# Kernel tuning notes

Measured on AMD Instinct MI355X. Metric: run time of the kernel, lower is better.

The kernel has to match this reference:

```python
import jax, jax.numpy as jnp
import numpy as np
import math

B, L, C, H, CP = 2, 512, 576, 8, 128
C3 = C // 3            # 192
DK = C // H            # 72
DK3 = DK // 3          # 24
DIV = math.sqrt(DK)


def _ln(x, w, b, eps=1e-6):
    m = jnp.mean(x, axis=-1, keepdims=True)
    v = jnp.mean(jnp.square(x - m), axis=-1, keepdims=True)
    return (x - m) * jax.lax.rsqrt(v + eps) * w + b


def setup_inputs() -> dict:
    key = jax.random.key(0)
    ks = jax.random.split(key, 12)
    s = 0.05
    def n(k, shape):
        return jax.random.normal(k, shape, jnp.float32) * s
    return {
        "x": jax.random.normal(ks[0], (B, L, C), jnp.float32),
        "pairX": jax.random.normal(ks[1], (B, L, L, CP), jnp.float32),
        "g": jnp.ones((1,), jnp.float32),
        "ln1_w": jnp.ones((C,), jnp.float32), "ln1_b": jnp.zeros((C,), jnp.float32),
        "ln2_w": jnp.ones((CP,), jnp.float32), "ln2_b": jnp.zeros((CP,), jnp.float32),
        "Wq": n(ks[2], (C3, C3)), "bq": jnp.zeros((C3,), jnp.float32),
        "Wk": n(ks[3], (C3, C3)), "bk": jnp.zeros((C3,), jnp.float32),
        "Wv": n(ks[4], (C3, C3)), "bv": jnp.zeros((C3,), jnp.float32),
        "Wg": n(ks[5], (C3, C3)), "bg": jnp.zeros((C3,), jnp.float32),
        "conv_w": n(ks[6], (3, H, H, 5, 5)), "conv_b": jnp.zeros((3, H), jnp.float32),
        "Wp": n(ks[7], (CP, H)), "bp": jnp.zeros((H,), jnp.float32),
        "Wpr": n(ks[8], (H, CP)), "bpr": jnp.zeros((CP,), jnp.float32),
        "Wo": n(ks[9], (C, C)), "bo": jnp.zeros((C,), jnp.float32),
    }


def reference(x, pairX, g, ln1_w, ln1_b, ln2_w, ln2_b, Wq, bq, Wk, bk, Wv, bv,
              Wg, bg, conv_w, conv_b, Wp, bp, Wpr, bpr, Wo, bo):
    ori_x = x
    xn = _ln(x, ln1_w, ln1_b)                      # [B,L,C]
    pn = _ln(pairX, ln2_w, ln2_b)                  # [B,L,L,CP]

    # split channels into 3 groups: [B,3,L,C3]
    xs = xn.reshape(B, L, 3, C3).transpose(0, 2, 1, 3)

    def proj(W, b):
        y = xs @ W + b                              # [B,3,L,C3]
        return y.reshape(B, 3, L, H, DK3).transpose(0, 1, 3, 2, 4)  # [B,3,H,L,DK3]

    q = proj(Wq, bq)
    k = proj(Wk, bk)
    v = proj(Wv, bv)
    gate = proj(Wg, bg)

    qkMatrix = jnp.einsum('bchld,bchmd->bchlm', q, k)  # [B,3,H,L,L]
    pairBias = (pn @ Wp + bp).transpose(0, 3, 1, 2)[:, None]  # [B,1,H,L,L]
    oriQK = qkMatrix + pairBias                     # [B,3,H,L,L]

    # 3-channel 5x5 conv refinement, summed over the 3 branches -> [B,1,H,L,L]
    dn = ('NCHW', 'OIHW', 'NCHW')
    convQK = sum(
        jax.lax.conv_general_dilated(oriQK[:, i], conv_w[i], (1, 1), 'SAME',
                                     dimension_numbers=dn)
        + conv_b[i][None, :, None, None]
        for i in range(3)
    )[:, None]

    qk = (oriQK + convQK) / DIV                     # [B,3,H,L,L]
    score = jax.nn.softmax(qk, axis=-1)
    h_outs = jnp.einsum('bchlm,bchmd->bchld', score, v) * jax.nn.sigmoid(gate)
    h_outs = h_outs.transpose(0, 3, 1, 2, 4).reshape(B, L, C)

    rawScoreMean = jax.nn.gelu(jnp.mean(qk, axis=1).transpose(0, 2, 3, 1),
                               approximate=False)   # [B,L,L,H]
    out1 = (h_outs @ Wo + bo) + ori_x * g
    out2 = rawScoreMean @ Wpr + bpr                 # [B,L,L,CP]
    return out1, out2
```

## Files before the change

### kernel.cpp

```cpp
#include <hip/hip_runtime.h>
#include <hip/hip_bf16.h>

#define BDIM 2
#define LDIM 512
#define CDIM 576
#define HDIM 8
#define CPD  128
#define DK3  24
#define INV_DIV 0.117851130197757920f

static constexpr size_t OFF_Q    = 0;
static constexpr size_t OFF_K    = 589824;
static constexpr size_t OFF_V    = 1179648;
static constexpr size_t OFF_G    = 1769472;
static constexpr size_t OFF_BIAS = 2359296;
static constexpr size_t OFF_ORI  = OFF_BIAS + 4194304;
static constexpr size_t OFF_QK   = OFF_ORI + 12582912;
static constexpr size_t OFF_H    = OFF_QK + 12582912;
static constexpr size_t OFF_WPH  = OFF_H + 589824;
static constexpr size_t OFF_CS   = OFF_WPH + 1024;
static constexpr size_t OFF_XN   = OFF_QK;

__device__ __forceinline__ float gelu_exact(float v) {
    return 0.5f * v * (1.f + erff(v * 0.70710678118654752f));
}

typedef float __attribute__((ext_vector_type(4))) f32x4;
__device__ __forceinline__ void nt_store4(float* p, float a, float b, float c, float d) {
    f32x4 t = {a, b, c, d};
    __builtin_nontemporal_store(t, (f32x4*)p);
}

__global__ __launch_bounds__(256) void k_prep(
    const float* __restrict__ ln2w, const float* __restrict__ ln2b,
    const float* __restrict__ Wp, const float* __restrict__ bp,
    float* __restrict__ wph, float* __restrict__ csum)
{
    __shared__ float wl[1024];
    const int tid = threadIdx.x;
    for (int i = tid; i < 1024; i += 256) {
        int h = i >> 7, d = i & 127;
        float v = ln2w[d] * Wp[d * 8 + h];
        wl[i] = v; wph[i] = v;
    }
    __syncthreads();
    const int h = tid >> 5, c4 = tid & 31;
    float p = wl[h * 128 + c4 * 4] + wl[h * 128 + c4 * 4 + 1]
            + wl[h * 128 + c4 * 4 + 2] + wl[h * 128 + c4 * 4 + 3];
#pragma unroll
    for (int o = 1; o < 32; o <<= 1) p += __shfl_xor(p, o);
    if (c4 == 0) csum[h] = p;
    float q = 0.f;
#pragma unroll
    for (int k = 0; k < 4; ++k) { int d = c4 * 4 + k; q = fmaf(ln2b[d], Wp[d * 8 + h], q); }
#pragma unroll
    for (int o = 1; o < 32; o <<= 1) q += __shfl_xor(q, o);
    if (c4 == 0) csum[8 + h] = q + bp[h];
}

__global__ __launch_bounds__(256) void k_ln(
    const float* __restrict__ x, const float* __restrict__ ln1w, const float* __restrict__ ln1b,
    float* __restrict__ xn)
{
    const int tid = threadIdx.x;
    const int wid = tid >> 6, lane = tid & 63;
    const int row = blockIdx.x * 4 + wid;
    const float* xr = x + (size_t)row * CDIM;
    float vals[9]; float s = 0.f, sq = 0.f;
#pragma unroll
    for (int u = 0; u < 9; ++u) {
        float v = xr[lane + 64 * u];
        vals[u] = v; s += v; sq += v * v;
    }
#pragma unroll
    for (int o = 32; o; o >>= 1) { s += __shfl_xor(s, o); sq += __shfl_xor(sq, o); }
    float m = s * (1.f / 576.f);
    float inv = rsqrtf(sq * (1.f / 576.f) - m * m + 1e-6f);
    float* xo = xn + (size_t)row * CDIM;
#pragma unroll
    for (int u = 0; u < 9; ++u) {
        int idx = lane + 64 * u;
        xo[idx] = (vals[u] - m) * inv * ln1w[idx] + ln1b[idx];
    }
}

__global__ __launch_bounds__(256) void k_proj(
    const float* __restrict__ xn,
    const float* __restrict__ Wq, const float* __restrict__ bq,
    const float* __restrict__ Wk, const float* __restrict__ bk,
    const float* __restrict__ Wv, const float* __restrict__ bv,
    const float* __restrict__ Wg, const float* __restrict__ bg,
    float* __restrict__ qo, float* __restrict__ ko, float* __restrict__ vo, float* __restrict__ go)
{
    __shared__ float As[192 * 64];
    __shared__ float Bs[32 * 192];
    const int tid = threadIdx.x;
    const int bx = blockIdx.x;
    const int mi = bx / 48, rem = bx % 48;
    const int g = rem >> 4, rb = rem & 15;
    const int row0 = rb * 64;

    const float* W  = mi == 0 ? Wq : mi == 1 ? Wk : mi == 2 ? Wv : Wg;
    const float* bb = mi == 0 ? bq : mi == 1 ? bk : mi == 2 ? bv : bg;
    float* op       = mi == 0 ? qo : mi == 1 ? ko : mi == 2 ? vo : go;

    {
        const int r = tid & 63, k4b = tid >> 6;
#pragma unroll
        for (int it = 0; it < 12; ++it) {
            int k4 = k4b + it * 4;
            float4 v = *(const float4*)&xn[(size_t)(row0 + r) * 576 + g * 192 + k4 * 4];
            As[(k4 * 4 + 0) * 64 + r] = v.x;
            As[(k4 * 4 + 1) * 64 + r] = v.y;
            As[(k4 * 4 + 2) * 64 + r] = v.z;
            As[(k4 * 4 + 3) * 64 + r] = v.w;
        }
    }

    const int rg = tid >> 4, cg = tid & 15;
    const int r0 = rg * 4, c0 = cg * 12;
    float acc[4][12] = {};

    for (int kk = 0; kk < 192; kk += 32) {
        __syncthreads();
#pragma unroll
        for (int i = 0; i < 6; ++i) {
            int f = tid + 256 * i;
            int k2 = f / 48, c4 = f % 48;
            *(float4*)&Bs[k2 * 192 + c4 * 4] = *(const float4*)&W[(size_t)(kk + k2) * 192 + c4 * 4];
        }
        __syncthreads();
#pragma unroll
        for (int k2 = 0; k2 < 32; ++k2) {
            const float4 a  = *(const float4*)&As[(kk + k2) * 64 + r0];
            const float4 b0 = *(const float4*)&Bs[k2 * 192 + c0];
            const float4 b1 = *(const float4*)&Bs[k2 * 192 + c0 + 4];
            const float4 b2 = *(const float4*)&Bs[k2 * 192 + c0 + 8];
            const float ar[4] = {a.x, a.y, a.z, a.w};
#pragma unroll
            for (int r = 0; r < 4; ++r) {
                acc[r][0] = fmaf(ar[r], b0.x, acc[r][0]);
                acc[r][1] = fmaf(ar[r], b0.y, acc[r][1]);
                acc[r][2] = fmaf(ar[r], b0.z, acc[r][2]);
                acc[r][3] = fmaf(ar[r], b0.w, acc[r][3]);
                acc[r][4] = fmaf(ar[r], b1.x, acc[r][4]);
                acc[r][5] = fmaf(ar[r], b1.y, acc[r][5]);
                acc[r][6] = fmaf(ar[r], b1.z, acc[r][6]);
                acc[r][7] = fmaf(ar[r], b1.w, acc[r][7]);
                acc[r][8] = fmaf(ar[r], b2.x, acc[r][8]);
                acc[r][9] = fmaf(ar[r], b2.y, acc[r][9]);
                acc[r][10] = fmaf(ar[r], b2.z, acc[r][10]);
                acc[r][11] = fmaf(ar[r], b2.w, acc[r][11]);
            }
        }
    }

    const int h = cg >> 1, d24 = (cg & 1) * 12;
    const float4 bj0 = *(const float4*)&bb[c0];
    const float4 bj1 = *(const float4*)&bb[c0 + 4];
    const float4 bj2 = *(const float4*)&bb[c0 + 8];
#pragma unroll
    for (int r = 0; r < 4; ++r) {
        int row = row0 + r0 + r;
        int b = row >> 9, l = row & 511;
        float* o = op + ((((size_t)b * 3 + g) * HDIM + h) * LDIM + l) * DK3 + d24;
        *(float4*)(o + 0) = make_float4(acc[r][0] + bj0.x, acc[r][1] + bj0.y,
                                        acc[r][2] + bj0.z, acc[r][3] + bj0.w);
        *(float4*)(o + 4) = make_float4(acc[r][4] + bj1.x, acc[r][5] + bj1.y,
                                        acc[r][6] + bj1.z, acc[r][7] + bj1.w);
        *(float4*)(o + 8) = make_float4(acc[r][8] + bj2.x, acc[r][9] + bj2.y,
                                        acc[r][10] + bj2.z, acc[r][11] + bj2.w);
    }
}

__global__ __launch_bounds__(256) void k_pairbias(
    const float* __restrict__ pairX, const float* __restrict__ wph,
    const float* __restrict__ csum, float* __restrict__ bias)
{
    const int row = blockIdx.x * 256 + threadIdx.x;
    const float* rp = pairX + (size_t)row * CPD;

    float acc[8] = {};
    float sum = 0.f, sumsq = 0.f;
    for (int s = 0; s < 8; ++s) {
        float rr[16];
        *(float4*)&rr[0]  = *(const float4*)(rp + s * 16 + 0);
        *(float4*)&rr[4]  = *(const float4*)(rp + s * 16 + 4);
        *(float4*)&rr[8]  = *(const float4*)(rp + s * 16 + 8);
        *(float4*)&rr[12] = *(const float4*)(rp + s * 16 + 12);
#pragma unroll
        for (int k = 0; k < 16; ++k) { sum += rr[k]; sumsq = fmaf(rr[k], rr[k], sumsq); }
        const float* wp_s = wph + s * 16;
#pragma unroll
        for (int h = 0; h < 8; ++h) {
            const float* w = wp_s + h * 128;
#pragma unroll
            for (int k = 0; k < 16; ++k) acc[h] = fmaf(rr[k], w[k], acc[h]);
        }
    }
    const float m = sum * (1.f / 128.f);
    const float inv = rsqrtf(sumsq * (1.f / 128.f) - m * m + 1e-6f);
    const int b = row >> 18;
    const int ij = row & 262143;
    float* bo = bias + ((size_t)b << 21) + ij;
#pragma unroll
    for (int h = 0; h < 8; ++h) {
        float o = inv * (acc[h] - m * csum[h]) + csum[8 + h];
        bo[(size_t)h << 18] = o;
    }
}

__global__ __launch_bounds__(256) void k_qkmat(
    const float* __restrict__ q, const float* __restrict__ k,
    const float* __restrict__ bias, float* __restrict__ oriQK)
{
    __shared__ float Kl[512 * 28];
    __shared__ float Ql[32 * 28];
    const int tid = threadIdx.x;
    const int bch = blockIdx.x >> 4;
    const int itile = blockIdx.x & 15;
    const float* kp = k + (size_t)bch * 512 * 24;
    const float* qp = q + (size_t)bch * 512 * 24 + (size_t)itile * 32 * 24;
    for (int idx = tid; idx < 512 * 24; idx += 256) {
        int j = idx / 24, d = idx - j * 24;
        Kl[j * 28 + d] = kp[idx];
    }
    for (int idx = tid; idx < 32 * 24; idx += 256) {
        int i = idx / 24, d = idx - i * 24;
        Ql[i * 28 + d] = qp[idx];
    }
    __syncthreads();

    const int ti = tid >> 4, tj = tid & 15;
    const int b = bch / 24, h = bch & 7;
    const float* biasp = bias + ((size_t)(b * 8 + h) * 512 + itile * 32) * 512;
    float* outp = oriQK + (size_t)bch * 262144 + (size_t)itile * 32 * 512;

    for (int cc = 0; cc < 4; ++cc) {
        float acc[2][8] = {};
#pragma unroll
        for (int d4 = 0; d4 < 6; ++d4) {
            const float4 q0 = *(const float4*)&Ql[(ti * 2 + 0) * 28 + d4 * 4];
            const float4 q1 = *(const float4*)&Ql[(ti * 2 + 1) * 28 + d4 * 4];
#pragma unroll
            for (int u = 0; u < 8; ++u) {
                const float4 kv = *(const float4*)&Kl[(cc * 128 + u * 16 + tj) * 28 + d4 * 4];
                acc[0][u] = fmaf(q0.x, kv.x, fmaf(q0.y, kv.y, fmaf(q0.z, kv.z, fmaf(q0.w, kv.w, acc[0][u]))));
                acc[1][u] = fmaf(q1.x, kv.x, fmaf(q1.y, kv.y, fmaf(q1.z, kv.z, fmaf(q1.w, kv.w, acc[1][u]))));
            }
        }
#pragma unroll
        for (int r = 0; r < 2; ++r) {
            int i = ti * 2 + r;
#pragma unroll
            for (int u = 0; u < 8; ++u) {
                int j = cc * 128 + u * 16 + tj;
                outp[(size_t)i * 512 + j] = acc[r][u] + biasp[(size_t)i * 512 + j];
            }
        }
    }
}

__global__ __launch_bounds__(256, 4) void k_conv(
    const float* __restrict__ oriQK, const float* __restrict__ convW, const float* __restrict__ convB,
    const float* __restrict__ Wpr, const float* __restrict__ bpr,
    float* __restrict__ qk, float* __restrict__ out2)
{
    __shared__ float tile[8 * 36 * 24];
    __shared__ float wT[1600];
    const int tid = threadIdx.x;
    const int bx = blockIdx.x;
    const int b = bx >> 9, rem = bx & 511;
    const int i0 = (rem >> 5) * 32, j0 = (rem & 31) * 16;

    const int jg = tid & 7, ii = tid >> 3;
    const int j2 = jg * 2;
    float acc[8][2] = {};

    for (int c = 0; c < 3; ++c) {
        __syncthreads();
        for (int i = tid; i < 1600; i += 256) {
            int h = i & 7, rest = i >> 3;
            int tap = rest % 25, hi = rest / 25;
            wT[hi * 200 + tap * 8 + h] = convW[c * 1600 + h * 200 + hi * 25 + tap];
        }
        for (int idx = tid; idx < 8 * 720; idx += 256) {
            int ch = idx / 720;
            int r = idx - ch * 720;
            int iw = r / 20, jw = r - iw * 20;
            int gi = i0 - 2 + iw, gj = j0 - 2 + jw;
            float v = 0.f;
            if ((unsigned)gi < 512u && (unsigned)gj < 512u)
                v = oriQK[((size_t)(b * 24 + c * 8 + ch) << 18) + ((size_t)gi << 9) + gj];
            tile[ch * 864 + iw * 24 + jw] = v;
        }
        __syncthreads();

        for (int hi = 0; hi < 8; ++hi) {
            const float* tch = &tile[hi * 864];
            const float* wch = &wT[hi * 200];
#pragma unroll
            for (int kh = 0; kh < 5; ++kh) {
                const float* trow = &tch[(ii + kh) * 24 + j2];
                float v[6];
                *(float2*)&v[0] = *(const float2*)&trow[0];
                *(float2*)&v[2] = *(const float2*)&trow[2];
                *(float2*)&v[4] = *(const float2*)&trow[4];
#pragma unroll
                for (int kw = 0; kw < 5; ++kw) {
                    const float4 wA = *(const float4*)&wch[(kh * 5 + kw) * 8];
                    const float4 wB = *(const float4*)&wch[(kh * 5 + kw) * 8 + 4];
#pragma unroll
                    for (int j = 0; j < 2; ++j) {
                        float vv = v[kw + j];
                        acc[0][j] = fmaf(wA.x, vv, acc[0][j]);
                        acc[1][j] = fmaf(wA.y, vv, acc[1][j]);
                        acc[2][j] = fmaf(wA.z, vv, acc[2][j]);
                        acc[3][j] = fmaf(wA.w, vv, acc[3][j]);
                        acc[4][j] = fmaf(wB.x, vv, acc[4][j]);
                        acc[5][j] = fmaf(wB.y, vv, acc[5][j]);
                        acc[6][j] = fmaf(wB.z, vv, acc[6][j]);
                        acc[7][j] = fmaf(wB.w, vv, acc[7][j]);
                    }
                }
            }
        }
    }

    const int gi = i0 + ii, gj = j0 + j2;
    const float* orib = oriQK + ((size_t)(b * 24) << 18) + ((size_t)gi << 9) + gj;
    float* qkb = qk + ((size_t)(b * 24) << 18) + ((size_t)gi << 9) + gj;
#pragma unroll
    for (int h = 0; h < 8; ++h) {
        float cv = convB[h] + convB[8 + h] + convB[16 + h];
        float cj0 = acc[h][0] + cv, cj1 = acc[h][1] + cv;
        float mm0 = 0.f, mm1 = 0.f;
#pragma unroll
        for (int c = 0; c < 3; ++c) {
            const float2 t = *(const float2*)(orib + ((size_t)(c * 8 + h) << 18));
            mm0 += t.x; mm1 += t.y;
            float2 o = make_float2((t.x + cj0) * INV_DIV, (t.y + cj1) * INV_DIV);
            *(float2*)(qkb + ((size_t)(c * 8 + h) << 18)) = o;
        }
        acc[h][0] = gelu_exact((mm0 * (1.f / 3.f) + cj0) * INV_DIV);
        acc[h][1] = gelu_exact((mm1 * (1.f / 3.f) + cj1) * INV_DIV);
    }
    __syncthreads();

    float* gql = tile;
#pragma unroll
    for (int h = 0; h < 8; ++h)
        *(float2*)&gql[h * 512 + ii * 16 + j2] = make_float2(acc[h][0], acc[h][1]);
    __syncthreads();

    const int pq = tid & 31, pg = tid >> 5;
    float4 wv[8];
#pragma unroll
    for (int h = 0; h < 8; ++h) wv[h] = *(const float4*)&Wpr[h * 128 + pq * 4];
    const float4 bv = *(const float4*)&bpr[pq * 4];

    for (int it = 0; it < 64; ++it) {
        int pos = it * 8 + pg;
        float g8[8];
#pragma unroll
        for (int h = 0; h < 8; ++h) g8[h] = gql[h * 512 + pos];
        float ox = bv.x + g8[0]*wv[0].x + g8[1]*wv[1].x + g8[2]*wv[2].x + g8[3]*wv[3].x
                 + g8[4]*wv[4].x + g8[5]*wv[5].x + g8[6]*wv[6].x + g8[7]*wv[7].x;
        float oy = bv.y + g8[0]*wv[0].y + g8[1]*wv[1].y + g8[2]*wv[2].y + g8[3]*wv[3].y
                 + g8[4]*wv[4].y + g8[5]*wv[5].y + g8[6]*wv[6].y + g8[7]*wv[7].y;
        float oz = bv.z + g8[0]*wv[0].z + g8[1]*wv[1].z + g8[2]*wv[2].z + g8[3]*wv[3].z
                 + g8[4]*wv[4].z + g8[5]*wv[5].z + g8[6]*wv[6].z + g8[7]*wv[7].z;
        float ow = bv.w + g8[0]*wv[0].w + g8[1]*wv[1].w + g8[2]*wv[2].w + g8[3]*wv[3].w
                 + g8[4]*wv[4].w + g8[5]*wv[5].w + g8[6]*wv[6].w + g8[7]*wv[7].w;
        int oi = i0 + (pos >> 4), oj = j0 + (pos & 15);
        nt_store4(&out2[(((size_t)(b * 512 + oi) << 9) + oj) * 128 + pq * 4], ox, oy, oz, ow);
    }
}

__global__ __launch_bounds__(256) void k_softmax_pv(
    const float* __restrict__ qk, const float* __restrict__ v, const float* __restrict__ gate,
    float* __restrict__ houts)
{
    __shared__ float Vl[512 * 28];
    const int tid = threadIdx.x;
    const int bch = blockIdx.x >> 4, itile = blockIdx.x & 15;
    const float* vp = v + (size_t)bch * (512 * 24);
    for (int idx = tid; idx < 512 * 24; idx += 256) {
        int j = idx / 24, d = idx - j * 24;
        Vl[j * 28 + d] = vp[idx];
    }
    __syncthreads();

    const int wid = tid >> 6, lane = tid & 63;
    const int b = bch / 24, c = (bch % 24) >> 3, h = bch & 7;
    const int tg = lane >> 3;
    for (int rr = 0; rr < 8; ++rr) {
        const int i = itile * 32 + wid * 8 + rr;
        const float* row = qk + ((size_t)bch * 512 + i) * 512;
        float e[8]; float mx = -1e30f;
#pragma unroll
        for (int u = 0; u < 8; ++u) { e[u] = row[lane + 64 * u]; mx = fmaxf(mx, e[u]); }
#pragma unroll
        for (int o = 32; o; o >>= 1) mx = fmaxf(mx, __shfl_xor(mx, o));
        float s = 0.f;
#pragma unroll
        for (int u = 0; u < 8; ++u) { e[u] = __expf(e[u] - mx); s += e[u]; }
#pragma unroll
        for (int o = 32; o; o >>= 1) s += __shfl_xor(s, o);
        float inv = 1.f / s;

        float4 a4[6] = {};
#pragma unroll
        for (int u = 0; u < 8; ++u) {
            float p = e[u] * inv;
            const float* vr = &Vl[(u * 64 + lane) * 28];
#pragma unroll
            for (int k = 0; k < 6; ++k) {
                float4 vv = *(const float4*)(vr + 4 * k);
                a4[k].x = fmaf(p, vv.x, a4[k].x);
                a4[k].y = fmaf(p, vv.y, a4[k].y);
                a4[k].z = fmaf(p, vv.z, a4[k].z);
                a4[k].w = fmaf(p, vv.w, a4[k].w);
            }
        }
#pragma unroll
        for (int k = 0; k < 6; ++k) {
            a4[k].x += __shfl_xor(a4[k].x, 8);  a4[k].y += __shfl_xor(a4[k].y, 8);
            a4[k].z += __shfl_xor(a4[k].z, 8);  a4[k].w += __shfl_xor(a4[k].w, 8);
            a4[k].x += __shfl_xor(a4[k].x, 16); a4[k].y += __shfl_xor(a4[k].y, 16);
            a4[k].z += __shfl_xor(a4[k].z, 16); a4[k].w += __shfl_xor(a4[k].w, 16);
            a4[k].x += __shfl_xor(a4[k].x, 32); a4[k].y += __shfl_xor(a4[k].y, 32);
            a4[k].z += __shfl_xor(a4[k].z, 32); a4[k].w += __shfl_xor(a4[k].w, 32);
        }
        const float af[24] = {
            a4[0].x, a4[0].y, a4[0].z, a4[0].w, a4[1].x, a4[1].y, a4[1].z, a4[1].w,
            a4[2].x, a4[2].y, a4[2].z, a4[2].w, a4[3].x, a4[3].y, a4[3].z, a4[3].w,
            a4[4].x, a4[4].y, a4[4].z, a4[4].w, a4[5].x, a4[5].y, a4[5].z, a4[5].w };
        float w0 = tg==0?af[0]:tg==1?af[3]:tg==2?af[6]:tg==3?af[9]:tg==4?af[12]:tg==5?af[15]:tg==6?af[18]:af[21];
        float w1 = tg==0?af[1]:tg==1?af[4]:tg==2?af[7]:tg==3?af[10]:tg==4?af[13]:tg==5?af[16]:tg==6?af[19]:af[22];
        float w2 = tg==0?af[2]:tg==1?af[5]:tg==2?af[8]:tg==3?af[11]:tg==4?af[14]:tg==5?af[17]:tg==6?af[20]:af[23];
#pragma unroll
        for (int o = 1; o < 8; o <<= 1) {
            w0 += __shfl_xor(w0, o);
            w1 += __shfl_xor(w1, o);
            w2 += __shfl_xor(w2, o);
        }
        if ((lane & 7) == 0) {
            const int d0 = tg * 3;
            const float* gp = gate + ((size_t)bch * 512 + i) * 24 + d0;
            float* op = houts + ((size_t)(b * 512 + i)) * 576 + c * 192 + h * 24 + d0;
            op[0] = w0 / (1.f + __expf(-gp[0]));
            op[1] = w1 / (1.f + __expf(-gp[1]));
            op[2] = w2 / (1.f + __expf(-gp[2]));
        }
    }
}

__global__ __launch_bounds__(256) void k_out1(
    const float* __restrict__ houts, const float* __restrict__ Wo, const float* __restrict__ bo,
    const float* __restrict__ x, const float* __restrict__ gsc,
    float* __restrict__ out1)
{
    __shared__ float As[32 * 33];
    __shared__ float Bs[32 * 64];
    const int tid = threadIdx.x;
    const int mt = blockIdx.x / 9, nt = blockIdx.x % 9;
    const int m0 = mt * 32, n0 = nt * 64;
    const int tn = tid & 15, tm = tid >> 4;
    float acc[2][4] = {};

    for (int kk = 0; kk < 576; kk += 32) {
        {
            int idx = tid;
#pragma unroll
            for (int i = 0; i < 4; ++i, idx += 256) {
                int k2 = idx & 31, m = idx >> 5;
                As[m * 33 + k2] = houts[(size_t)(m0 + m) * 576 + kk + k2];
            }
        }
        {
            int idx = tid;
#pragma unroll
            for (int i = 0; i < 8; ++i, idx += 256) {
                int n = idx & 63, k2 = idx >> 6;
                Bs[k2 * 64 + n] = Wo[(size_t)(kk + k2) * 576 + n0 + n];
            }
        }
        __syncthreads();
#pragma unroll
        for (int k2 = 0; k2 < 32; ++k2) {
            float a0 = As[(tm * 2 + 0) * 33 + k2];
            float a1 = As[(tm * 2 + 1) * 33 + k2];
            const float4 bv = *(const float4*)&Bs[k2 * 64 + tn * 4];
            acc[0][0] += a0 * bv.x; acc[0][1] += a0 * bv.y; acc[0][2] += a0 * bv.z; acc[0][3] += a0 * bv.w;
            acc[1][0] += a1 * bv.x; acc[1][1] += a1 * bv.y; acc[1][2] += a1 * bv.z; acc[1][3] += a1 * bv.w;
        }
        __syncthreads();
    }

    const float gv = gsc[0];
    const float4 b4 = *(const float4*)&bo[n0 + tn * 4];
#pragma unroll
    for (int r = 0; r < 2; ++r) {
        size_t row = (size_t)m0 + tm * 2 + r;
        size_t off = row * 576 + n0 + tn * 4;
        const float4 x4 = *(const float4*)&x[off];
        nt_store4(&out1[off],
                  acc[r][0] + b4.x + x4.x * gv,
                  acc[r][1] + b4.y + x4.y * gv,
                  acc[r][2] + b4.z + x4.z * gv,
                  acc[r][3] + b4.w + x4.w * gv);
    }
}

extern "C" void kernel_launch(void* const* d_in, const int* in_sizes, int n_in,
                              void* d_out, int out_size, void* d_ws, size_t ws_size,
                              hipStream_t stream) {
    const float* x     = (const float*)d_in[0];
    const float* pairX = (const float*)d_in[1];
    const float* g     = (const float*)d_in[2];
    const float* ln1w  = (const float*)d_in[3];
    const float* ln1b  = (const float*)d_in[4];
    const float* ln2w  = (const float*)d_in[5];
    const float* ln2b  = (const float*)d_in[6];
    const float* Wq    = (const float*)d_in[7];
    const float* bq    = (const float*)d_in[8];
    const float* Wk    = (const float*)d_in[9];
    const float* bk    = (const float*)d_in[10];
    const float* Wv    = (const float*)d_in[11];
    const float* bv    = (const float*)d_in[12];
    const float* Wg    = (const float*)d_in[13];
    const float* bg    = (const float*)d_in[14];
    const float* convW = (const float*)d_in[15];
    const float* convB = (const float*)d_in[16];
    const float* Wp    = (const float*)d_in[17];
    const float* bp    = (const float*)d_in[18];
    const float* Wpr   = (const float*)d_in[19];
    const float* bpr   = (const float*)d_in[20];
    const float* Wo    = (const float*)d_in[21];
    const float* bo    = (const float*)d_in[22];

    float* ws   = (float*)d_ws;
    float* q    = ws + OFF_Q;
    float* k    = ws + OFF_K;
    float* vv   = ws + OFF_V;
    float* gt   = ws + OFF_G;
    float* bias = ws + OFF_BIAS;
    float* ori  = ws + OFF_ORI;
    float* qkb  = ws + OFF_QK;
    float* xn   = ws + OFF_XN;
    float* hout = ws + OFF_H;
    float* wph  = ws + OFF_WPH;
    float* csum = ws + OFF_CS;

    float* out1 = (float*)d_out;
    float* out2 = out1 + 589824;

    k_prep<<<dim3(1), dim3(256), 0, stream>>>(ln2w, ln2b, Wp, bp, wph, csum);
    k_ln<<<dim3(256), dim3(256), 0, stream>>>(x, ln1w, ln1b, xn);
    k_proj<<<dim3(192), dim3(256), 0, stream>>>(xn, Wq, bq, Wk, bk, Wv, bv, Wg, bg,
                                                q, k, vv, gt);
    k_pairbias<<<dim3(2048), dim3(256), 0, stream>>>(pairX, wph, csum, bias);
    k_qkmat<<<dim3(768), dim3(256), 0, stream>>>(q, k, bias, ori);
    k_conv<<<dim3(1024), dim3(256), 0, stream>>>(ori, convW, convB, Wpr, bpr, qkb, out2);
    k_softmax_pv<<<dim3(768), dim3(256), 0, stream>>>(qkb, vv, gt, hout);
    k_out1<<<dim3(288), dim3(256), 0, stream>>>(hout, Wo, bo, x, g, out1);
}
```

Before: 415.7 us.

## Defer qk materialization: store conv sum only and recompute logits in softmax

The conv kernel no longer writes the full 3-branch scaled qk tensor or re-reads oriQK from global memory. It takes the centre values for the branch mean from the shared tile it already loaded, and writes only the branch-summed conv output, which is a third of the size, into the now-dead pair-bias buffer. The softmax kernel rebuilds the logits as (ori + convsum) * 1/sqrt(dk) on load. This cuts global memory traffic, at the cost of an extra stream read in softmax and reliance on the bias buffer being dead after the qk-matrix kernel.

Result: slower. 424.4 us (+2.1%).

```diff
diff --git a/kernel.cpp b/kernel.cpp
--- a/kernel.cpp
+++ b/kernel.cpp
@@ -264,7 +264,7 @@
 __global__ __launch_bounds__(256, 4) void k_conv(
     const float* __restrict__ oriQK, const float* __restrict__ convW, const float* __restrict__ convB,
     const float* __restrict__ Wpr, const float* __restrict__ bpr,
-    float* __restrict__ qk, float* __restrict__ out2)
+    float* __restrict__ convsum, float* __restrict__ out2)
 {
     __shared__ float tile[8 * 36 * 24];
     __shared__ float wT[1600];
@@ -276,6 +276,7 @@
     const int jg = tid & 7, ii = tid >> 3;
     const int j2 = jg * 2;
     float acc[8][2] = {};
+    float mm[8][2] = {};
 
     for (int c = 0; c < 3; ++c) {
         __syncthreads();
@@ -325,25 +326,23 @@
                 }
             }
         }
+#pragma unroll
+        for (int h = 0; h < 8; ++h) {
+            const float* tr = &tile[h * 864 + (ii + 2) * 24 + j2 + 2];
+            mm[h][0] += tr[0];
+            mm[h][1] += tr[1];
+        }
     }
 
     const int gi = i0 + ii, gj = j0 + j2;
-    const float* orib = oriQK + ((size_t)(b * 24) << 18) + ((size_t)gi << 9) + gj;
-    float* qkb = qk + ((size_t)(b * 24) << 18) + ((size_t)gi << 9) + gj;
+    float* csb = convsum + ((size_t)(b * 8) << 18) + ((size_t)gi << 9) + gj;
 #pragma unroll
     for (int h = 0; h < 8; ++h) {
         float cv = convB[h] + convB[8 + h] + convB[16 + h];
         float cj0 = acc[h][0] + cv, cj1 = acc[h][1] + cv;
-        float mm0 = 0.f, mm1 = 0.f;
-#pragma unroll
-        for (int c = 0; c < 3; ++c) {
-            const float2 t = *(const float2*)(orib + ((size_t)(c * 8 + h) << 18));
-            mm0 += t.x; mm1 += t.y;
-            float2 o = make_float2((t.x + cj0) * INV_DIV, (t.y + cj1) * INV_DIV);
-            *(float2*)(qkb + ((size_t)(c * 8 + h) << 18)) = o;
-        }
-        acc[h][0] = gelu_exact((mm0 * (1.f / 3.f) + cj0) * INV_DIV);
-        acc[h][1] = gelu_exact((mm1 * (1.f / 3.f) + cj1) * INV_DIV);
+        *(float2*)(csb + ((size_t)h << 18)) = make_float2(cj0, cj1);
+        acc[h][0] = gelu_exact((mm[h][0] * (1.f / 3.f) + cj0) * INV_DIV);
+        acc[h][1] = gelu_exact((mm[h][1] * (1.f / 3.f) + cj1) * INV_DIV);
     }
     __syncthreads();
 
@@ -378,7 +377,8 @@
 }
 
 __global__ __launch_bounds__(256) void k_softmax_pv(
-    const float* __restrict__ qk, const float* __restrict__ v, const float* __restrict__ gate,
+    const float* __restrict__ ori, const float* __restrict__ convsum,
+    const float* __restrict__ v, const float* __restrict__ gate,
     float* __restrict__ houts)
 {
     __shared__ float Vl[512 * 28];
@@ -396,10 +396,14 @@
     const int tg = lane >> 3;
     for (int rr = 0; rr < 8; ++rr) {
         const int i = itile * 32 + wid * 8 + rr;
-        const float* row = qk + ((size_t)bch * 512 + i) * 512;
+        const float* row = ori + ((size_t)bch * 512 + i) * 512;
+        const float* csr = convsum + ((size_t)(b * 8 + h) * 512 + i) * 512;
         float e[8]; float mx = -1e30f;
 #pragma unroll
-        for (int u = 0; u < 8; ++u) { e[u] = row[lane + 64 * u]; mx = fmaxf(mx, e[u]); }
+        for (int u = 0; u < 8; ++u) {
+            e[u] = (row[lane + 64 * u] + csr[lane + 64 * u]) * INV_DIV;
+            mx = fmaxf(mx, e[u]);
+        }
 #pragma unroll
         for (int o = 32; o; o >>= 1) mx = fmaxf(mx, __shfl_xor(mx, o));
         float s = 0.f;
@@ -546,8 +550,8 @@
     float* vv   = ws + OFF_V;
     float* gt   = ws + OFF_G;
     float* bias = ws + OFF_BIAS;
+    float* csb  = ws + OFF_BIAS;
     float* ori  = ws + OFF_ORI;
-    float* qkb  = ws + OFF_QK;
     float* xn   = ws + OFF_XN;
     float* hout = ws + OFF_H;
     float* wph  = ws + OFF_WPH;
@@ -562,7 +566,7 @@
                                                 q, k, vv, gt);
     k_pairbias<<<dim3(2048), dim3(256), 0, stream>>>(pairX, wph, csum, bias);
     k_qkmat<<<dim3(768), dim3(256), 0, stream>>>(q, k, bias, ori);
-    k_conv<<<dim3(1024), dim3(256), 0, stream>>>(ori, convW, convB, Wpr, bpr, qkb, out2);
-    k_softmax_pv<<<dim3(768), dim3(256), 0, stream>>>(qkb, vv, gt, hout);
+    k_conv<<<dim3(1024), dim3(256), 0, stream>>>(ori, convW, convB, Wpr, bpr, csb, out2);
+    k_softmax_pv<<<dim3(768), dim3(256), 0, stream>>>(ori, csb, vv, gt, hout);
     k_out1<<<dim3(288), dim3(256), 0, stream>>>(hout, Wo, bo, x, g, out1);
 }
```
